# Performance work log

Hardware: AMD Instinct MI355X
Metric: run time of the kernel (lower is better)

## Reference

```python
import jax, jax.numpy as jnp
import numpy as np

MODEL_DIM = 768
EMB_DIM = 768
NUM_HEADS = 12
HEAD_DIM = MODEL_DIM // NUM_HEADS  # 64
B, S = 4, 1024
LN_EPS = 1e-12


def setup_inputs() -> dict:
    key = jax.random.key(0)
    ks = jax.random.split(key, 12)
    s_in = 1.0 / np.sqrt(EMB_DIM)
    s_dm = 1.0 / np.sqrt(MODEL_DIM)
    return {
        "x": jax.random.normal(ks[0], (B, S, EMB_DIM), dtype=jnp.float32),
        # stacked per-head projection weights, [H, E, Dh] (in, out layout)
        "Wq": jax.random.normal(ks[1], (NUM_HEADS, EMB_DIM, HEAD_DIM), dtype=jnp.float32) * s_in,
        "bq": jax.random.normal(ks[2], (NUM_HEADS, HEAD_DIM), dtype=jnp.float32) * 0.02,
        "Wk": jax.random.normal(ks[3], (NUM_HEADS, EMB_DIM, HEAD_DIM), dtype=jnp.float32) * s_in,
        "bk": jax.random.normal(ks[4], (NUM_HEADS, HEAD_DIM), dtype=jnp.float32) * 0.02,
        "Wv": jax.random.normal(ks[5], (NUM_HEADS, EMB_DIM, HEAD_DIM), dtype=jnp.float32) * s_in,
        "bv": jax.random.normal(ks[6], (NUM_HEADS, HEAD_DIM), dtype=jnp.float32) * 0.02,
        # output dense [Dm, Dm] (in, out) + bias
        "Wd": jax.random.normal(ks[7], (MODEL_DIM, MODEL_DIM), dtype=jnp.float32) * s_dm,
        "bd": jax.random.normal(ks[8], (MODEL_DIM,), dtype=jnp.float32) * 0.02,
        # LayerNorm affine params
        "gamma": jnp.ones((MODEL_DIM,), dtype=jnp.float32),
        "beta": jnp.zeros((MODEL_DIM,), dtype=jnp.float32),
    }


def reference(x, Wq, bq, Wk, bk, Wv, bv, Wd, bd, gamma, beta):
    # Batched per-head projections: [B,S,E] x [H,E,Dh] -> [B,H,S,Dh]
    Q = jnp.einsum("bse,hed->bhsd", x, Wq) + bq[None, :, None, :]
    K = jnp.einsum("bse,hed->bhsd", x, Wk) + bk[None, :, None, :]
    V = jnp.einsum("bse,hed->bhsd", x, Wv) + bv[None, :, None, :]

    scale = 1.0 / jnp.sqrt(jnp.asarray(HEAD_DIM, dtype=Q.dtype))
    scores = jnp.einsum("bhsd,bhtd->bhst", Q, K) * scale  # [B,H,S,S]
    weights = jax.nn.softmax(scores, axis=-1)
    ctx = jnp.einsum("bhst,bhtd->bhsd", weights, V)  # [B,H,S,Dh]

    # concat per-head outputs along last dim (head order): [B,S,H*Dh]
    outputs = jnp.transpose(ctx, (0, 2, 1, 3)).reshape(B, S, NUM_HEADS * HEAD_DIM)
    # concat per-head attention weights along last dim: [B,S,H*S]
    weights_cat = jnp.transpose(weights, (0, 2, 1, 3)).reshape(B, S, NUM_HEADS * S)

    # BertSelfOutput: dense -> LayerNorm (dropout = identity in eval)
    y = jnp.einsum("bsi,io->bso", outputs, Wd) + bd
    mu = jnp.mean(y, axis=-1, keepdims=True)
    var = jnp.mean(jnp.square(y - mu), axis=-1, keepdims=True)
    y = (y - mu) * jax.lax.rsqrt(var + LN_EPS) * gamma + beta
    return weights_cat, y
```

## Files before the change

### kernel.cpp

```cpp
#include <hip/hip_runtime.h>

typedef __bf16 bf16x8 __attribute__((ext_vector_type(8)));
typedef __bf16 bf16x4 __attribute__((ext_vector_type(4)));
typedef float  f32x4  __attribute__((ext_vector_type(4)));
typedef unsigned short u16x8 __attribute__((ext_vector_type(8)));
typedef unsigned short u16x4 __attribute__((ext_vector_type(4)));

__device__ __forceinline__ unsigned short f2bf(float f) {
  union { float f; unsigned u; } v; v.f = f;
  unsigned r = v.u + 0x7fffu + ((v.u >> 16) & 1u);
  return (unsigned short)(r >> 16);
}

__device__ __forceinline__ float bf2f(unsigned short b) {
  union { unsigned u; float f; } v; v.u = (unsigned)b << 16;
  return v.f;
}

__device__ __forceinline__ void gload16(const unsigned short* g, unsigned short* l) {
  __builtin_amdgcn_global_load_lds(
      (const __attribute__((address_space(1))) unsigned int*)g,
      (__attribute__((address_space(3))) unsigned int*)l,
      16, 0, 0);
}

__device__ __forceinline__ void nt_store4(float* p, f32x4 v) {
  __builtin_nontemporal_store(v, (f32x4*)p);
}

#define WOFF 50331648
#define QSCALE 0.18033688011112042f

__device__ __forceinline__ int eidx(int row, int col) {
  return row * 1024 + ((((col >> 3) ^ (row & 7)) << 3) | (col & 7));
}

__global__ __launch_bounds__(256) void prep(
    const float* __restrict__ x, const float* __restrict__ Wq, const float* __restrict__ Wk,
    const float* __restrict__ Wv, const float* __restrict__ Wd,
    unsigned short* __restrict__ xb, unsigned short* __restrict__ wb, unsigned short* __restrict__ wdb)
{
  __shared__ float t[32][33];
  const int bid = blockIdx.x, tid = threadIdx.x;
  if (bid < 1536) {
    int i = (bid * 256 + tid) * 8;
    f32x4 v0 = *(const f32x4*)&x[i];
    f32x4 v1 = *(const f32x4*)&x[i + 4];
    u16x8 o;
    for (int j = 0; j < 4; j++) { o[j] = f2bf(v0[j]); o[j + 4] = f2bf(v1[j]); }
    *(u16x8*)&xb[i] = o;
    return;
  }
  const int tx = tid & 31, ty = tid >> 5;
  if (bid < 3264) {
    int q = bid - 1536;
    int bx = q & 1; q >>= 1;
    int by = q % 24, zz = q / 24;
    int m = zz / 12;
    const float* in = (m == 0 ? Wq : m == 1 ? Wk : Wv) + (long)(zz % 12) * 49152;
    unsigned short* ob = wb + (long)zz * 49152;
    int c = bx * 32 + tx, r0 = by * 32;
    for (int i = ty; i < 32; i += 8) t[i][tx] = in[(long)(r0 + i) * 64 + c];
    __syncthreads();
    int c0 = bx * 32;
    for (int i = ty; i < 32; i += 8) ob[(long)(c0 + i) * 768 + r0 + tx] = f2bf(t[tx][i]);
    return;
  }
  {
    int q = bid - 3264;
    int bx = q % 24, by = q / 24;
    int c = bx * 32 + tx, r0 = by * 32;
    for (int i = ty; i < 32; i += 8) t[i][tx] = Wd[(long)(r0 + i) * 768 + c];
    __syncthreads();
    int c0 = bx * 32;
    for (int i = ty; i < 32; i += 8) wdb[(long)(c0 + i) * 768 + r0 + tx] = f2bf(t[tx][i]);
  }
}

__global__ __launch_bounds__(256) void qkv_gemm(
    const unsigned short* __restrict__ xb, const unsigned short* __restrict__ wb,
    const float* __restrict__ bq, const float* __restrict__ bk, const float* __restrict__ bv,
    unsigned short* __restrict__ Qb, unsigned short* __restrict__ Kb, unsigned short* __restrict__ Vt)
{
  __shared__ unsigned short As[2][4096];
  __shared__ unsigned short Bs[2][4096];
  const int tid = threadIdx.x;
  const int bid = blockIdx.x;
  const int swz = (bid & 7) * 72 + (bid >> 3);
  const int bn = (swz % 18) * 128, bm = (swz / 18) * 128;
  const int w = tid >> 6, l = tid & 63;
  const int wr = w >> 1, wc = w & 1;
  const int lr = l & 15, lg = l >> 4;
  const int lofs = w << 9;

  f32x4 acc[4][4];
  for (int i = 0; i < 4; i++) for (int j = 0; j < 4; j++) acc[i][j] = {0.f, 0.f, 0.f, 0.f};

  const unsigned short* ga = xb + (long)(bm + (tid >> 2)) * 768 + (tid & 3) * 8;
  const unsigned short* gb = wb + (long)(bn + (tid >> 2)) * 768 + (tid & 3) * 8;

  gload16(ga,            &As[0][lofs]);
  gload16(ga + 64 * 768, &As[0][lofs + 2048]);
  gload16(gb,            &Bs[0][lofs]);
  gload16(gb + 64 * 768, &Bs[0][lofs + 2048]);
  __syncthreads();

  int cur = 0;
  for (int t = 0; t < 24; t++) {
    if (t < 23) {
      int k0 = (t + 1) * 32;
      gload16(ga + k0,            &As[cur ^ 1][lofs]);
      gload16(ga + k0 + 64 * 768, &As[cur ^ 1][lofs + 2048]);
      gload16(gb + k0,            &Bs[cur ^ 1][lofs]);
      gload16(gb + k0 + 64 * 768, &Bs[cur ^ 1][lofs + 2048]);
    }
    bf16x8 af[4], bfv[4];
    for (int i = 0; i < 4; i++) af[i]  = *(const bf16x8*)&As[cur][(wr * 64 + i * 16 + lr) * 32 + lg * 8];
    for (int j = 0; j < 4; j++) bfv[j] = *(const bf16x8*)&Bs[cur][(wc * 64 + j * 16 + lr) * 32 + lg * 8];
    for (int i = 0; i < 4; i++)
      for (int j = 0; j < 4; j++)
        acc[i][j] = __builtin_amdgcn_mfma_f32_16x16x32_bf16(af[i], bfv[j], acc[i][j], 0, 0, 0);
    __syncthreads();
    cur ^= 1;
  }

  for (int i = 0; i < 4; i++) for (int j = 0; j < 4; j++) {
    int col = bn + wc * 64 + j * 16 + lr;
    int m = col / 768, rc = col % 768;
    int h = rc >> 6, d = rc & 63;
    const float* bias = (m == 0) ? bq : (m == 1) ? bk : bv;
    float bb = bias[rc];
    for (int r = 0; r < 4; r++) {
      int row = bm + wr * 64 + i * 16 + lg * 4 + r;
      int b = row >> 10, s = row & 1023;
      float v = acc[i][j][r] + bb;
      if (m == 0)      Qb[((b * 12 + h) << 16) + (s << 6) + d] = f2bf(v * QSCALE);
      else if (m == 1) Kb[((b * 12 + h) << 16) + (s << 6) + d] = f2bf(v);
      else             Vt[((b * 12 + h) << 16) + (d << 10) + s] = f2bf(v);
    }
  }
}

__global__ __launch_bounds__(512, 4) void attn_kernel(
    const unsigned short* __restrict__ Qb, const unsigned short* __restrict__ Kb,
    const unsigned short* __restrict__ Vt,
    float* __restrict__ wout, unsigned short* __restrict__ ctx)
{
  extern __shared__ char smem[];
  unsigned short* E = (unsigned short*)smem;
  float* sred = (float*)(smem + 65536);

  const int bid = blockIdx.x;
  const int swz = (bid & 7) * 192 + (bid >> 3);
  const int bh = swz >> 5;
  const int q0 = (swz & 31) * 32;
  const int b = bh / 12, h = bh % 12;
  const int tid = threadIdx.x;
  const int w = tid >> 6, l = tid & 63, lr = l & 15, lg = l >> 4;
  const unsigned short* Qg = Qb + (bh << 16);
  const unsigned short* Kg = Kb + (bh << 16);
  const unsigned short* Vg = Vt + (bh << 16);

  bf16x8 qa[2][2];
#pragma unroll
  for (int ri = 0; ri < 2; ri++)
#pragma unroll
    for (int ks = 0; ks < 2; ks++)
      qa[ri][ks] = *(const bf16x8*)&Qg[(q0 + ri * 16 + lr) * 64 + ks * 32 + lg * 8];

  f32x4 sc[2][8];
#pragma unroll
  for (int cf = 0; cf < 8; cf++) {
    int colb = w * 128 + cf * 16;
    bf16x8 kb0 = *(const bf16x8*)&Kg[(colb + lr) * 64 + lg * 8];
    bf16x8 kb1 = *(const bf16x8*)&Kg[(colb + lr) * 64 + 32 + lg * 8];
#pragma unroll
    for (int ri = 0; ri < 2; ri++) {
      f32x4 a = {0.f, 0.f, 0.f, 0.f};
      a = __builtin_amdgcn_mfma_f32_16x16x32_bf16(kb0, qa[ri][0], a, 0, 0, 0);
      a = __builtin_amdgcn_mfma_f32_16x16x32_bf16(kb1, qa[ri][1], a, 0, 0, 0);
      sc[ri][cf] = a;
    }
  }

  float sm[2] = {0.f, 0.f};
#pragma unroll
  for (int cf = 0; cf < 8; cf++)
#pragma unroll
    for (int ri = 0; ri < 2; ri++) {
      bf16x4 pk;
#pragma unroll
      for (int r = 0; r < 4; r++) {
        float e = exp2f(sc[ri][cf][r]);
        sm[ri] += e;
        pk[r] = (__bf16)e;
      }
      *(bf16x4*)&E[eidx(ri * 16 + lr, w * 128 + cf * 16 + lg * 4)] = pk;
    }
#pragma unroll
  for (int ri = 0; ri < 2; ri++) {
    float s = sm[ri];
    s += __shfl_xor(s, 16);
    s += __shfl_xor(s, 32);
    if (lg == 0) sred[w * 32 + ri * 16 + lr] = s;
  }

  __syncthreads();

  float s_acc = 0.f;
  {
    int row_l = l & 31;
#pragma unroll
    for (int ww = 0; ww < 8; ww++) s_acc += sred[ww * 32 + row_l];
  }
  const float sfin_r = 1.f / s_acc;

  if (w < 4) {
    const int ri = w >> 1, cfp = (w & 1) * 2;
    f32x4 acc0 = {0.f, 0.f, 0.f, 0.f};
    f32x4 acc1 = {0.f, 0.f, 0.f, 0.f};
    __builtin_amdgcn_s_setprio(1);
#pragma unroll
    for (int ks = 0; ks < 32; ks++) {
      int kk = ks * 32;
      bf16x8 pa  = *(const bf16x8*)&E[eidx(ri * 16 + lr, kk + lg * 8)];
      bf16x8 vb0 = *(const bf16x8*)&Vg[(cfp * 16 + lr) * 1024 + kk + lg * 8];
      bf16x8 vb1 = *(const bf16x8*)&Vg[((cfp + 1) * 16 + lr) * 1024 + kk + lg * 8];
      acc0 = __builtin_amdgcn_mfma_f32_16x16x32_bf16(pa, vb0, acc0, 0, 0, 0);
      acc1 = __builtin_amdgcn_mfma_f32_16x16x32_bf16(pa, vb1, acc1, 0, 0, 0);
    }
    __builtin_amdgcn_s_setprio(0);
#pragma unroll
    for (int r = 0; r < 4; r++) {
      int row = ri * 16 + lg * 4 + r;
      float sf = __shfl(sfin_r, row);
      long base = (long)(b * 1024 + q0 + row) * 768 + h * 64;
      ctx[base + cfp * 16 + lr]       = f2bf(acc0[r] * sf);
      ctx[base + (cfp + 1) * 16 + lr] = f2bf(acc1[r] * sf);
    }
  } else {
    const int t = tid - 256;
    float* wbase = wout + (long)(b * 1024 + q0) * 12288 + h * 1024;
#pragma unroll
    for (int row = 0; row < 32; row++) {
      float sf = __shfl(sfin_r, row);
      int c4 = t * 4;
      u16x4 ev = *(const u16x4*)&E[eidx(row, c4)];
      f32x4 o;
      for (int j = 0; j < 4; j++) o[j] = bf2f(ev[j]) * sf;
      *(f32x4*)&wbase[(long)row * 12288 + c4] = o;
    }
  }
}

__global__ __launch_bounds__(256) void dense_gemm(
    const unsigned short* __restrict__ ctx, const unsigned short* __restrict__ wdb,
    const float* __restrict__ bd, float* __restrict__ y)
{
  __shared__ unsigned short As[2][2048];
  __shared__ unsigned short Bs[2][4096];
  const int tid = threadIdx.x;
  const int bid = blockIdx.x;
  const int swz = (bid & 7) * 48 + (bid >> 3);
  const int bn = (swz % 6) * 128, bm = (swz / 6) * 64;
  const int w = tid >> 6, l = tid & 63;
  const int wr = w >> 1, wc = w & 1;
  const int lr = l & 15, lg = l >> 4;
  const int lofs = w << 9;

  f32x4 acc[2][4];
  for (int i = 0; i < 2; i++) for (int j = 0; j < 4; j++) acc[i][j] = {0.f, 0.f, 0.f, 0.f};

  const unsigned short* ga = ctx + (long)(bm + (tid >> 2)) * 768 + (tid & 3) * 8;
  const unsigned short* gb = wdb + (long)(bn + (tid >> 2)) * 768 + (tid & 3) * 8;

  gload16(ga,            &As[0][lofs]);
  gload16(gb,            &Bs[0][lofs]);
  gload16(gb + 64 * 768, &Bs[0][lofs + 2048]);
  __syncthreads();

  int cur = 0;
  for (int t = 0; t < 24; t++) {
    if (t < 23) {
      int k0 = (t + 1) * 32;
      gload16(ga + k0,            &As[cur ^ 1][lofs]);
      gload16(gb + k0,            &Bs[cur ^ 1][lofs]);
      gload16(gb + k0 + 64 * 768, &Bs[cur ^ 1][lofs + 2048]);
    }
    bf16x8 af[2], bfv[4];
    for (int i = 0; i < 2; i++) af[i]  = *(const bf16x8*)&As[cur][(wr * 32 + i * 16 + lr) * 32 + lg * 8];
    for (int j = 0; j < 4; j++) bfv[j] = *(const bf16x8*)&Bs[cur][(wc * 64 + j * 16 + lr) * 32 + lg * 8];
    for (int i = 0; i < 2; i++)
      for (int j = 0; j < 4; j++)
        acc[i][j] = __builtin_amdgcn_mfma_f32_16x16x32_bf16(af[i], bfv[j], acc[i][j], 0, 0, 0);
    __syncthreads();
    cur ^= 1;
  }

  for (int i = 0; i < 2; i++) for (int j = 0; j < 4; j++) {
    int col = bn + wc * 64 + j * 16 + lr;
    float bb = bd[col];
    for (int r = 0; r < 4; r++) {
      int row = bm + wr * 32 + i * 16 + lg * 4 + r;
      y[(long)row * 768 + col] = acc[i][j][r] + bb;
    }
  }
}

__global__ __launch_bounds__(256) void ln_kernel(
    const float* __restrict__ y,
    const float* __restrict__ gamma, const float* __restrict__ beta,
    float* __restrict__ out)
{
  int w = threadIdx.x >> 6, l = threadIdx.x & 63;
  long row = blockIdx.x * 4 + w;
  const float* yr = y + row * 768;
  f32x4 v[3];
  float s = 0.f, ss = 0.f;
  for (int j = 0; j < 3; j++) {
    int c = j * 256 + l * 4;
    f32x4 t = *(const f32x4*)&yr[c];
    for (int q = 0; q < 4; q++) { s += t[q]; ss += t[q] * t[q]; }
    v[j] = t;
  }
  for (int o = 32; o >= 1; o >>= 1) { s += __shfl_xor(s, o); ss += __shfl_xor(ss, o); }
  float mu = s * (1.f / 768.f);
  float var = ss * (1.f / 768.f) - mu * mu;
  float rs = rsqrtf(var + 1e-12f);
  float* orow = out + row * 768;
  for (int j = 0; j < 3; j++) {
    int c = j * 256 + l * 4;
    f32x4 g = *(const f32x4*)&gamma[c];
    f32x4 be = *(const f32x4*)&beta[c];
    f32x4 o;
    for (int q = 0; q < 4; q++) o[q] = (v[j][q] - mu) * rs * g[q] + be[q];
    nt_store4(&orow[c], o);
  }
}

extern "C" void kernel_launch(void* const* d_in, const int* in_sizes, int n_in,
                              void* d_out, int out_size, void* d_ws, size_t ws_size,
                              hipStream_t stream) {
  const float* x     = (const float*)d_in[0];
  const float* Wq    = (const float*)d_in[1];
  const float* bq    = (const float*)d_in[2];
  const float* Wk    = (const float*)d_in[3];
  const float* bk    = (const float*)d_in[4];
  const float* Wv    = (const float*)d_in[5];
  const float* bv    = (const float*)d_in[6];
  const float* Wd    = (const float*)d_in[7];
  const float* bd    = (const float*)d_in[8];
  const float* gamma = (const float*)d_in[9];
  const float* beta  = (const float*)d_in[10];
  float* out = (float*)d_out;

  char* ws = (char*)d_ws;
  unsigned short* xb  = (unsigned short*)(ws);
  unsigned short* wb  = (unsigned short*)(ws + 6291456);
  unsigned short* wdb = (unsigned short*)(ws + 9830400);
  unsigned short* Qb  = (unsigned short*)(ws + 11010048);
  unsigned short* Kb  = (unsigned short*)(ws + 17301504);
  unsigned short* Vt  = (unsigned short*)(ws + 23592960);
  unsigned short* ctx = (unsigned short*)(ws + 29884416);
  float*          yws = (float*)(ws + 11010048);

  prep<<<3840, 256, 0, stream>>>(x, Wq, Wk, Wv, Wd, xb, wb, wdb);
  qkv_gemm<<<576, 256, 0, stream>>>(xb, wb, bq, bk, bv, Qb, Kb, Vt);
  attn_kernel<<<1536, 512, 66560, stream>>>(Qb, Kb, Vt, out, ctx);
  dense_gemm<<<384, 256, 0, stream>>>(ctx, wdb, bd, yws);
  ln_kernel<<<1024, 256, 0, stream>>>(yws, gamma, beta, out + WOFF);
}
```

Baseline: 157.0 us.

## Write attention weights from fp32 registers and split PV MFMA across all waves

Each wave now keeps its exp'd scores in fp32 registers and writes the normalized attention-weight output straight from them, instead of re-reading bf16 values from LDS in four dedicated waves. The P·V product is split so all eight waves each compute one 16x16 output tile, rather than four waves computing two tiles each. This drops an LDS round trip, gives fp32 precision on the weights output, and balances MFMA work across waves. The cost is that every wave now issues strided global stores, and the wave priority hint is removed.

```diff
diff --git a/kernel.cpp b/kernel.cpp
--- a/kernel.cpp
+++ b/kernel.cpp
@@ -193,6 +193,7 @@
       for (int r = 0; r < 4; r++) {
         float e = exp2f(sc[ri][cf][r]);
         sm[ri] += e;
+        sc[ri][cf][r] = e;
         pk[r] = (__bf16)e;
       }
       *(bf16x4*)&E[eidx(ri * 16 + lr, w * 128 + cf * 16 + lg * 4)] = pk;
@@ -214,41 +215,40 @@
     for (int ww = 0; ww < 8; ww++) s_acc += sred[ww * 32 + row_l];
   }
   const float sfin_r = 1.f / s_acc;
-
-  if (w < 4) {
-    const int ri = w >> 1, cfp = (w & 1) * 2;
-    f32x4 acc0 = {0.f, 0.f, 0.f, 0.f};
-    f32x4 acc1 = {0.f, 0.f, 0.f, 0.f};
-    __builtin_amdgcn_s_setprio(1);
+  const float sf0 = __shfl(sfin_r, lr);
+  const float sf1 = __shfl(sfin_r, 16 + lr);
+
+  {
+    float* wbase = wout + (long)(b * 1024 + q0) * 12288 + h * 1024;
+#pragma unroll
+    for (int ri = 0; ri < 2; ri++) {
+      float sf = ri ? sf1 : sf0;
+      long rowb = (long)(ri * 16 + lr) * 12288;
+#pragma unroll
+      for (int cf = 0; cf < 8; cf++) {
+        int col = w * 128 + cf * 16 + lg * 4;
+        f32x4 o = sc[ri][cf];
+        o[0] *= sf; o[1] *= sf; o[2] *= sf; o[3] *= sf;
+        *(f32x4*)&wbase[rowb + col] = o;
+      }
+    }
+  }
+
+  {
+    const int ri = w >> 2, cf = w & 3;
+    f32x4 acc = {0.f, 0.f, 0.f, 0.f};
 #pragma unroll
     for (int ks = 0; ks < 32; ks++) {
       int kk = ks * 32;
-      bf16x8 pa  = *(const bf16x8*)&E[eidx(ri * 16 + lr, kk + lg * 8)];
-      bf16x8 vb0 = *(const bf16x8*)&Vg[(cfp * 16 + lr) * 1024 + kk + lg * 8];
-      bf16x8 vb1 = *(const bf16x8*)&Vg[((cfp + 1) * 16 + lr) * 1024 + kk + lg * 8];
-      acc0 = __builtin_amdgcn_mfma_f32_16x16x32_bf16(pa, vb0, acc0, 0, 0, 0);
-      acc1 = __builtin_amdgcn_mfma_f32_16x16x32_bf16(pa, vb1, acc1, 0, 0, 0);
-    }
-    __builtin_amdgcn_s_setprio(0);
+      bf16x8 pa = *(const bf16x8*)&E[eidx(ri * 16 + lr, kk + lg * 8)];
+      bf16x8 vb = *(const bf16x8*)&Vg[(cf * 16 + lr) * 1024 + kk + lg * 8];
+      acc = __builtin_amdgcn_mfma_f32_16x16x32_bf16(pa, vb, acc, 0, 0, 0);
+    }
 #pragma unroll
     for (int r = 0; r < 4; r++) {
       int row = ri * 16 + lg * 4 + r;
       float sf = __shfl(sfin_r, row);
-      long base = (long)(b * 1024 + q0 + row) * 768 + h * 64;
-      ctx[base + cfp * 16 + lr]       = f2bf(acc0[r] * sf);
-      ctx[base + (cfp + 1) * 16 + lr] = f2bf(acc1[r] * sf);
-    }
-  } else {
-    const int t = tid - 256;
-    float* wbase = wout + (long)(b * 1024 + q0) * 12288 + h * 1024;
-#pragma unroll
-    for (int row = 0; row < 32; row++) {
-      float sf = __shfl(sfin_r, row);
-      int c4 = t * 4;
-      u16x4 ev = *(const u16x4*)&E[eidx(row, c4)];
-      f32x4 o;
-      for (int j = 0; j < 4; j++) o[j] = bf2f(ev[j]) * sf;
-      *(f32x4*)&wbase[(long)row * 12288 + c4] = o;
+      ctx[(long)(b * 1024 + q0 + row) * 768 + h * 64 + cf * 16 + lr] = f2bf(acc[r] * sf);
     }
   }
 }
```

New measurement: 162.4 us. 1.03x slower.
